# Kernel optimization log

Measured on AMD Instinct MI355X. Metric: run time of the kernel, lower is better.

## Reference

```python
import jax, jax.numpy as jnp
import numpy as np

NUM_HEADS = 8
NUM_GROUPS = 32
EPS = 1e-5


def group_norm(x, gamma, beta):
    b, c, h, w = x.shape
    xg = x.reshape(b, NUM_GROUPS, c // NUM_GROUPS, h, w)
    mean = jnp.mean(xg, axis=(2, 3, 4), keepdims=True)
    var = jnp.var(xg, axis=(2, 3, 4), keepdims=True)
    xn = ((xg - mean) * jax.lax.rsqrt(var + EPS)).reshape(b, c, h, w)
    return xn * gamma[None, :, None, None] + beta[None, :, None, None]


def setup_inputs() -> dict:
    key = jax.random.key(0)
    ks = jax.random.split(key, 4)
    b, c, h, w = 16, 512, 32, 32
    x = jax.random.normal(ks[0], (b, c, h, w), dtype=jnp.float32)
    gn_gamma = jnp.ones((c,), dtype=jnp.float32)
    gn_beta = jnp.zeros((c,), dtype=jnp.float32)
    qkv_w = jax.random.normal(ks[1], (3 * c, c), dtype=jnp.float32) * (1.0 / np.sqrt(c))
    qkv_b = jnp.zeros((3 * c,), dtype=jnp.float32)
    proj_w = jax.random.normal(ks[2], (c, c), dtype=jnp.float32) * (1.0 / np.sqrt(c))
    proj_b = jnp.zeros((c,), dtype=jnp.float32)
    return {"x": x, "gn_gamma": gn_gamma, "gn_beta": gn_beta,
            "qkv_w": qkv_w, "qkv_b": qkv_b, "proj_w": proj_w, "proj_b": proj_b}


def reference(x, gn_gamma, gn_beta, qkv_w, qkv_b, proj_w, proj_b):
    b, c, h, w = x.shape
    hd = c // NUM_HEADS
    hw = h * w

    xn = group_norm(x, gn_gamma, gn_beta)
    # 1x1 conv == channel matmul
    qkv = jnp.einsum('oc,bchw->bohw', qkv_w, xn) + qkv_b[None, :, None, None]
    q, k, v = jnp.split(qkv, 3, axis=1)
    q = q.reshape(b, NUM_HEADS, hd, hw)
    k = k.reshape(b, NUM_HEADS, hd, hw)
    v = v.reshape(b, NUM_HEADS, hd, hw)

    scale = 1.0 / np.sqrt(hd)
    attn = jnp.einsum('bhdt,bhds->bhts', q, k) * scale  # [b,H,hw,hw]
    attn = jax.nn.softmax(attn, axis=-1)
    h_attn = jnp.einsum('bhts,bhds->bhdt', attn, v).reshape(b, c, h, w)

    h_attn = jnp.einsum('oc,bchw->bohw', proj_w, h_attn) + proj_b[None, :, None, None]
    return x + h_attn
```

## Files before the change

### kernel.cpp

```cpp
#include <hip/hip_runtime.h>
#include <math.h>

#define NUM_HEADS 8
#define NUM_GROUPS 32
#define EPS 1e-5f

constexpr int B  = 16;
constexpr int C  = 512;
constexpr int HW = 1024;
constexpr int HD = 64;

typedef short bf16x8 __attribute__((ext_vector_type(8)));
typedef float f32x4  __attribute__((ext_vector_type(4)));

#define QSCALE 0.1803368801111f

__device__ inline unsigned short f2bf(float f) {
    union { float f; unsigned int u; } v; v.f = f;
    unsigned int r = (v.u + 0x7FFFu + ((v.u >> 16) & 1u)) >> 16;
    return (unsigned short)r;
}

__device__ __forceinline__ unsigned int pack_trunc(float lo, float hi) {
    return __builtin_amdgcn_perm(__float_as_uint(hi), __float_as_uint(lo), 0x07060302u);
}

__device__ __forceinline__ float exp2_raw(float x) {
#if __has_builtin(__builtin_amdgcn_exp2f)
    return __builtin_amdgcn_exp2f(x);
#else
    float r; asm("v_exp_f32 %0, %1" : "=v"(r) : "v"(x)); return r;
#endif
}

__device__ __forceinline__ void gld_lds16(void* lds, const void* g) {
    __builtin_amdgcn_global_load_lds(
        (const __attribute__((address_space(1))) void*)g,
        (__attribute__((address_space(3))) void*)lds, 16, 0, 0);
}

__device__ __forceinline__ void pl32_swap(unsigned int& a, unsigned int& b) {
#if __has_builtin(__builtin_amdgcn_permlane32_swap)
    auto r = __builtin_amdgcn_permlane32_swap(a, b, false, false);
    a = r[0]; b = r[1];
#else
    asm volatile("v_permlane32_swap_b32 %0, %1" : "+v"(a), "+v"(b));
#endif
}
__device__ __forceinline__ void pl16_swap(unsigned int& a, unsigned int& b) {
#if __has_builtin(__builtin_amdgcn_permlane16_swap)
    auto r = __builtin_amdgcn_permlane16_swap(a, b, false, false);
    a = r[0]; b = r[1];
#else
    asm volatile("v_permlane16_swap_b32 %0, %1" : "+v"(a), "+v"(b));
#endif
}

__global__ __launch_bounds__(256)
void groupnorm_t_kernel(const float* __restrict__ x,
                        const float* __restrict__ gamma,
                        const float* __restrict__ beta,
                        unsigned short* __restrict__ xnT) {
    const int bg = blockIdx.x;
    const int b = bg >> 5, g = bg & 31;
    const size_t base = ((size_t)b * C + (size_t)g * 16) * HW;

    float v[4][16];
    float sum = 0.f, sumsq = 0.f;
    #pragma unroll
    for (int p = 0; p < 4; ++p) {
        const int t = threadIdx.x + p * 256;
        #pragma unroll
        for (int cl = 0; cl < 16; ++cl) {
            const float f = x[base + (size_t)cl * HW + t];
            v[p][cl] = f;
            sum += f;
            sumsq += f * f;
        }
    }
    #pragma unroll
    for (int off = 32; off > 0; off >>= 1) {
        sum   += __shfl_down(sum, off, 64);
        sumsq += __shfl_down(sumsq, off, 64);
    }
    __shared__ float s_sum[4], s_sq[4];
    const int wid = threadIdx.x >> 6, lane = threadIdx.x & 63;
    if (lane == 0) { s_sum[wid] = sum; s_sq[wid] = sumsq; }
    __syncthreads();
    const float tsum = s_sum[0] + s_sum[1] + s_sum[2] + s_sum[3];
    const float tsq  = s_sq[0] + s_sq[1] + s_sq[2] + s_sq[3];
    const float mean = tsum * (1.0f / 16384.f);
    const float var  = tsq * (1.0f / 16384.f) - mean * mean;
    const float rstd = rsqrtf(var + EPS);

    float ga[16], be[16];
    #pragma unroll
    for (int cl = 0; cl < 16; ++cl) {
        ga[cl] = gamma[g * 16 + cl] * rstd;
        be[cl] = beta[g * 16 + cl] - mean * ga[cl];
    }

    #pragma unroll
    for (int p = 0; p < 4; ++p) {
        const int t = threadIdx.x + p * 256;
        unsigned short pk[16];
        #pragma unroll
        for (int cl = 0; cl < 16; ++cl)
            pk[cl] = f2bf(v[p][cl] * ga[cl] + be[cl]);
        unsigned short* dst = xnT + ((size_t)(b * 1024 + t)) * 512 + g * 16;
        *(uint4*)dst = *(const uint4*)pk;
        *(uint4*)(dst + 8) = *(const uint4*)(pk + 8);
    }
}

__global__ __launch_bounds__(256)
void wconv_kernel(const float* __restrict__ qkv_w,
                  const float* __restrict__ proj_w,
                  unsigned short* __restrict__ wqb) {
    const int i = blockIdx.x * 256 + threadIdx.x;
    const int n1 = 786432 / 4;
    const int nt = 1048576 / 4;
    if (i >= nt) return;
    const float4 v = (i < n1) ? ((const float4*)qkv_w)[i]
                              : ((const float4*)proj_w)[i - n1];
    ushort4 r;
    r.x = f2bf(v.x); r.y = f2bf(v.y); r.z = f2bf(v.z); r.w = f2bf(v.w);
    ((ushort4*)wqb)[i] = r;
}

__device__ __forceinline__ void mfma_gemm_core(const char* __restrict__ Ab,
                                               const char* __restrict__ Bb,
                                               unsigned short* As,
                                               unsigned short* Bs,
                                               f32x4 acc[4][4]) {
    const int tid = threadIdx.x;
    const int w = tid >> 6, lane = tid & 63;
    const int lo = lane & 15, q4 = lane >> 4;
    const int wm = w >> 1, wn = w & 1;
    const int lrow = lane >> 2, lkc = lane & 3;

    for (int k0 = 0; k0 < 512; k0 += 32) {
        __syncthreads();
        #pragma unroll
        for (int i = 0; i < 2; ++i) {
            const int row = w * 32 + i * 16 + lrow;
            const int kc = lkc ^ ((row >> 1) & 3);
            const size_t goff = (size_t)row * 1024 + k0 * 2 + kc * 16;
            gld_lds16((char*)As + w * 2048 + i * 1024, Ab + goff);
            gld_lds16((char*)Bs + w * 2048 + i * 1024, Bb + goff);
        }
        __syncthreads();

        bf16x8 af[4], bfr[4];
        #pragma unroll
        for (int i = 0; i < 4; ++i) {
            const int ra = wm * 64 + i * 16 + lo;
            af[i]  = *(const bf16x8*)(As + ra * 32 + (q4 ^ ((ra >> 1) & 3)) * 8);
            const int rb = wn * 64 + i * 16 + lo;
            bfr[i] = *(const bf16x8*)(Bs + rb * 32 + (q4 ^ ((rb >> 1) & 3)) * 8);
        }
        #pragma unroll
        for (int mi = 0; mi < 4; ++mi)
            #pragma unroll
            for (int ni = 0; ni < 4; ++ni)
                acc[mi][ni] = __builtin_amdgcn_mfma_f32_16x16x32_bf16(
                    af[mi], bfr[ni], acc[mi][ni], 0, 0, 0);
    }
}

__global__ __launch_bounds__(256)
void qkv_mfma_kernel(const unsigned short* __restrict__ wqb,
                     const unsigned short* __restrict__ xnT,
                     const float* __restrict__ qkv_b,
                     unsigned short* __restrict__ Qt,
                     unsigned short* __restrict__ Kt,
                     unsigned short* __restrict__ Vb) {
    __shared__ __align__(16) unsigned short SMEM[8192];
    unsigned short* As = SMEM;
    unsigned short* Bs = SMEM + 4096;
    const int batch = blockIdx.z;
    const int mBase = blockIdx.y * 128, nBase = blockIdx.x * 128;

    f32x4 acc[4][4] = {};
    mfma_gemm_core((const char*)(wqb + (size_t)mBase * 512),
                   (const char*)(xnT + ((size_t)batch * 1024 + nBase) * 512),
                   As, Bs, acc);

    const int tid = threadIdx.x;
    const int w = tid >> 6, lane = tid & 63;
    const int lo = lane & 15, q4 = lane >> 4;
    const int wm = w >> 1, wn = w & 1;
    const int mw = mBase + wm * 64;
    const int tb = nBase + wn * 64;

    __syncthreads();

    if (mw < 1024) {
        const bool isQ = mw < 512;
        const int head = (mw >> 6) & 7;
        unsigned short* dst = (isQ ? Qt : Kt) + (((size_t)batch * 8 + head) << 16);
        const float sc = isQ ? QSCALE : 1.0f;
        #pragma unroll
        for (int mi = 0; mi < 4; ++mi) {
            const float4 bq = *(const float4*)(qkv_b + mw + mi * 16 + q4 * 4);
            #pragma unroll
            for (int ni = 0; ni < 4; ++ni) {
                const int t = tb + ni * 16 + lo;
                ushort4 pk;
                pk.x = f2bf((acc[mi][ni][0] + bq.x) * sc);
                pk.y = f2bf((acc[mi][ni][1] + bq.y) * sc);
                pk.z = f2bf((acc[mi][ni][2] + bq.z) * sc);
                pk.w = f2bf((acc[mi][ni][3] + bq.w) * sc);
                *(ushort4*)(dst + (size_t)t * 64 + mi * 16 + q4 * 4) = pk;
            }
        }
    } else {
        unsigned short* T = SMEM + w * 2048;
        unsigned short* Vrow = Vb + (size_t)batch * 524288 + (size_t)(mw - 1024) * 1024 + tb;
        const int rl8 = lane >> 3, c8 = lane & 7;
        #pragma unroll
        for (int p = 0; p < 2; ++p) {
            #pragma unroll
            for (int mi2 = 0; mi2 < 2; ++mi2) {
                const int mi = 2 * p + mi2;
                const float4 bq = *(const float4*)(qkv_b + mw + mi * 16 + q4 * 4);
                const int dl = mi2 * 16 + q4 * 4;
                #pragma unroll
                for (int ni = 0; ni < 4; ++ni) {
                    const int tl = ni * 16 + lo;
                    T[(dl + 0) * 64 + tl] = f2bf(acc[mi][ni][0] + bq.x);
                    T[(dl + 1) * 64 + tl] = f2bf(acc[mi][ni][1] + bq.y);
                    T[(dl + 2) * 64 + tl] = f2bf(acc[mi][ni][2] + bq.z);
                    T[(dl + 3) * 64 + tl] = f2bf(acc[mi][ni][3] + bq.w);
                }
            }
            #pragma unroll
            for (int i = 0; i < 4; ++i) {
                const int dl = i * 8 + rl8;
                const uint4 val = *(const uint4*)&T[dl * 64 + c8 * 8];
                *(uint4*)(Vrow + (size_t)(p * 32 + dl) * 1024 + c8 * 8) = val;
            }
        }
    }
}

__global__ __launch_bounds__(256, 4)
void attn_mfma_kernel(const unsigned short* __restrict__ Qt,
                      const unsigned short* __restrict__ Kt,
                      const unsigned short* __restrict__ Vb,
                      unsigned short* __restrict__ attnT) {
    const int bh = blockIdx.x;
    const int b = bh >> 3, h = bh & 7;
    const int tBase = blockIdx.y * 128;
    const int tid = threadIdx.x;
    const int w = tid >> 6, lane = tid & 63;
    const int lo = lane & 15, q4 = lane >> 4;
    const int xr = lo & 7;

    __shared__ __align__(16) unsigned short Ks[2][64 * 64];
    __shared__ __align__(16) unsigned short Vs[2][64 * 64];

    const unsigned short* Kp = Kt + ((size_t)bh << 16);
    const unsigned short* Vp = Vb + ((size_t)b * 512 + h * 64) * 1024;

    bf16x8 qf[2][2];
    {
        const unsigned short* Qp = Qt + ((size_t)bh * 1024 + tBase + 32 * w) * 64;
        #pragma unroll
        for (int nt = 0; nt < 2; ++nt) {
            qf[nt][0] = *(const bf16x8*)(Qp + (size_t)(16 * nt + lo) * 64 + 8 * q4);
            qf[nt][1] = *(const bf16x8*)(Qp + (size_t)(16 * nt + lo) * 64 + 32 + 8 * q4);
        }
    }

    const int rl = lane >> 3, p8 = lane & 7;
    auto stage = [&](int s0, unsigned short* Kd, unsigned short* Vd) {
        #pragma unroll
        for (int cc = 0; cc < 2; ++cc) {
            const int r = 16 * w + 8 * cc + rl;
            const int jj = p8 ^ (r & 7);
            gld_lds16(Kd + (16 * w + 8 * cc) * 64, Kp + (size_t)(s0 + r) * 64 + jj * 8);
            gld_lds16(Vd + (16 * w + 8 * cc) * 64, Vp + (size_t)r * 1024 + s0 + jj * 8);
        }
    };

    f32x4 oacc[4][2] = {};
    float lrun[2] = {0.f, 0.f};

    auto chunk = [&](const unsigned short* Kc, const unsigned short* Vc,
                     int s0next, unsigned short* KsN, unsigned short* VsN,
                     bool doStage) {
        __syncthreads();
        if (doStage) stage(s0next, KsN, VsN);

        f32x4 sacc[4][2] = {};
        __builtin_amdgcn_s_setprio(1);
        #pragma unroll
        for (int mt = 0; mt < 4; ++mt) {
            const unsigned short* kr = Kc + (16 * mt + lo) * 64;
            const bf16x8 a0 = *(const bf16x8*)(kr + ((q4    ) ^ xr) * 8);
            const bf16x8 a1 = *(const bf16x8*)(kr + ((q4 + 4) ^ xr) * 8);
            #pragma unroll
            for (int nt = 0; nt < 2; ++nt) {
                sacc[mt][nt] = __builtin_amdgcn_mfma_f32_16x16x32_bf16(a0, qf[nt][0], sacc[mt][nt], 0, 0, 0);
                sacc[mt][nt] = __builtin_amdgcn_mfma_f32_16x16x32_bf16(a1, qf[nt][1], sacc[mt][nt], 0, 0, 0);
            }
        }
        __builtin_amdgcn_s_setprio(0);

        bf16x8 bp[2][2];
        #pragma unroll
        for (int nt = 0; nt < 2; ++nt) {
            unsigned int X[4][2];
            float ps = 0.f;
            #pragma unroll
            for (int mt = 0; mt < 4; ++mt) {
                const f32x4 s = sacc[mt][nt];
                const float p0 = exp2_raw(s[0]);
                const float p1 = exp2_raw(s[1]);
                const float p2 = exp2_raw(s[2]);
                const float p3 = exp2_raw(s[3]);
                ps += (p0 + p1) + (p2 + p3);
                X[mt][0] = pack_trunc(p0, p1);
                X[mt][1] = pack_trunc(p2, p3);
            }
            lrun[nt] += ps;
            #pragma unroll
            for (int h2 = 0; h2 < 2; ++h2) {
                unsigned int Y0, Y1, Y2, Y3;
                {
                    unsigned int a = X[2 * h2][0], bb = X[2 * h2 + 1][0];
                    pl32_swap(a, bb);
                    pl16_swap(a, bb);
                    Y0 = a; Y2 = bb;
                }
                {
                    unsigned int a = X[2 * h2][1], bb = X[2 * h2 + 1][1];
                    pl32_swap(a, bb);
                    pl16_swap(a, bb);
                    Y1 = a; Y3 = bb;
                }
                union { unsigned int u[4]; bf16x8 v; } cv;
                cv.u[0] = Y0; cv.u[1] = Y1; cv.u[2] = Y2; cv.u[3] = Y3;
                bp[nt][h2] = cv.v;
            }
        }

        __builtin_amdgcn_s_setprio(1);
        #pragma unroll
        for (int md = 0; md < 4; ++md) {
            const unsigned short* vr = Vc + (16 * md + lo) * 64;
            const bf16x8 v0 = *(const bf16x8*)(vr + ((q4    ) ^ xr) * 8);
            const bf16x8 v1 = *(const bf16x8*)(vr + ((q4 + 4) ^ xr) * 8);
            #pragma unroll
            for (int nt = 0; nt < 2; ++nt) {
                oacc[md][nt] = __builtin_amdgcn_mfma_f32_16x16x32_bf16(v0, bp[nt][0], oacc[md][nt], 0, 0, 0);
                oacc[md][nt] = __builtin_amdgcn_mfma_f32_16x16x32_bf16(v1, bp[nt][1], oacc[md][nt], 0, 0, 0);
            }
        }
        __builtin_amdgcn_s_setprio(0);
    };

    stage(0, Ks[0], Vs[0]);

    #pragma unroll 1
    for (int ii = 0; ii < 8; ++ii) {
        chunk(Ks[0], Vs[0], (2 * ii + 1) * 64, Ks[1], Vs[1], true);
        chunk(Ks[1], Vs[1], (2 * ii + 2) * 64, Ks[0], Vs[0], ii < 7);
    }

    #pragma unroll
    for (int nt = 0; nt < 2; ++nt) {
        float lt = lrun[nt];
        lt += __shfl_xor(lt, 16, 64);
        lt += __shfl_xor(lt, 32, 64);
        const float inv = 1.0f / lt;
        const int t = tBase + 32 * w + 16 * nt + lo;
        unsigned short* op = attnT + ((size_t)(b * 1024 + t)) * 512 + h * 64;
        #pragma unroll
        for (int md = 0; md < 4; ++md) {
            uint2 pk;
            pk.x = pack_trunc(oacc[md][nt][0] * inv, oacc[md][nt][1] * inv);
            pk.y = pack_trunc(oacc[md][nt][2] * inv, oacc[md][nt][3] * inv);
            *(uint2*)(op + 16 * md + 4 * q4) = pk;
        }
    }
}

__global__ __launch_bounds__(256)
void proj_mfma_kernel(const unsigned short* __restrict__ wpb,
                      const unsigned short* __restrict__ attnT,
                      const float* __restrict__ proj_b,
                      const float* __restrict__ x,
                      float* __restrict__ out) {
    __shared__ __align__(16) unsigned short As[128 * 32];
    __shared__ __align__(16) unsigned short Bs[128 * 32];
    const int batch = blockIdx.z;
    const int mBase = blockIdx.y * 128, nBase = blockIdx.x * 128;

    f32x4 acc[4][4] = {};
    mfma_gemm_core((const char*)(wpb + (size_t)mBase * 512),
                   (const char*)(attnT + ((size_t)batch * 1024 + nBase) * 512),
                   As, Bs, acc);

    const int tid = threadIdx.x;
    const int w = tid >> 6, lane = tid & 63;
    const int lo = lane & 15, q4 = lane >> 4;
    const int wm = w >> 1, wn = w & 1;
    const float* xb = x + (size_t)batch * 524288;
    float* ob = out + (size_t)batch * 524288;

    #pragma unroll
    for (int mi = 0; mi < 4; ++mi) {
        const int m0 = mBase + wm * 64 + mi * 16 + q4 * 4;
        const float4 bq = *(const float4*)(proj_b + m0);
        #pragma unroll
        for (int ni = 0; ni < 4; ++ni) {
            const int t = nBase + wn * 64 + ni * 16 + lo;
            const size_t o0 = (size_t)m0 * 1024 + t;
            ob[o0]          = acc[mi][ni][0] + bq.x + xb[o0];
            ob[o0 + 1024]   = acc[mi][ni][1] + bq.y + xb[o0 + 1024];
            ob[o0 + 2048]   = acc[mi][ni][2] + bq.z + xb[o0 + 2048];
            ob[o0 + 3072]   = acc[mi][ni][3] + bq.w + xb[o0 + 3072];
        }
    }
}

extern "C" void kernel_launch(void* const* d_in, const int* in_sizes, int n_in,
                              void* d_out, int out_size, void* d_ws, size_t ws_size,
                              hipStream_t stream) {
    const float* x        = (const float*)d_in[0];
    const float* gn_gamma = (const float*)d_in[1];
    const float* gn_beta  = (const float*)d_in[2];
    const float* qkv_w    = (const float*)d_in[3];
    const float* qkv_b    = (const float*)d_in[4];
    const float* proj_w   = (const float*)d_in[5];
    const float* proj_b   = (const float*)d_in[6];
    float* out = (float*)d_out;

    char* wsc = (char*)d_ws;
    unsigned short* xnT   = (unsigned short*)(wsc);
    unsigned short* Qt    = (unsigned short*)(wsc + 16777216);
    unsigned short* Kt    = (unsigned short*)(wsc + 33554432);
    unsigned short* Vb    = (unsigned short*)(wsc + 50331648);
    unsigned short* attnT = (unsigned short*)(wsc + 67108864);
    unsigned short* wqb   = (unsigned short*)(wsc + 83886080);
    unsigned short* wpb   = wqb + 786432;

    groupnorm_t_kernel<<<B * NUM_GROUPS, 256, 0, stream>>>(x, gn_gamma, gn_beta, xnT);

    wconv_kernel<<<1024, 256, 0, stream>>>(qkv_w, proj_w, wqb);

    {
        dim3 grid(HW / 128, (3 * C) / 128, B);
        qkv_mfma_kernel<<<grid, 256, 0, stream>>>(wqb, xnT, qkv_b, Qt, Kt, Vb);
    }

    {
        dim3 grid(B * NUM_HEADS, HW / 128);
        attn_mfma_kernel<<<grid, 256, 0, stream>>>(Qt, Kt, Vb, attnT);
    }

    {
        dim3 grid(HW / 128, C / 128, B);
        proj_mfma_kernel<<<grid, 256, 0, stream>>>(wpb, attnT, proj_b, x, out);
    }
}
```

Measured before the change: 226.0 us.

## Triple-buffer K/V staging in attention with explicit vmcnt barriers

Converts the attention kernel's double-buffered K/V LDS pipeline into a three-stage ring, so loads for chunk i+2 are in flight while chunk i is computed. The plain __syncthreads is replaced with an inline-asm s_waitcnt vmcnt(N) plus s_barrier, so each wave waits only on the oldest outstanding direct-to-LDS loads rather than draining all of them. The aim is to hide global-load latency behind MFMA work. In exchange, LDS use per block grows by half and launch bounds drop from 4 to 3 blocks per CU, which may cost occupancy. The hard-coded vmcnt count must match the number of loads per stage.

Result: faster. 212.7 us (-5.9%).

```diff
diff --git a/kernel.cpp b/kernel.cpp
--- a/kernel.cpp
+++ b/kernel.cpp
@@ -55,6 +55,11 @@
     asm volatile("v_permlane16_swap_b32 %0, %1" : "+v"(a), "+v"(b));
 #endif
 }
+
+#define ABAR(VM) do {                                                   \
+    asm volatile("s_waitcnt vmcnt(" VM ")\n\ts_barrier" ::: "memory");  \
+    __builtin_amdgcn_sched_barrier(0);                                  \
+} while (0)
 
 __global__ __launch_bounds__(256)
 void groupnorm_t_kernel(const float* __restrict__ x,
@@ -244,7 +249,94 @@
     }
 }
 
-__global__ __launch_bounds__(256, 4)
+__device__ __forceinline__ void attn_stage(const unsigned short* __restrict__ Kp,
+                                           const unsigned short* __restrict__ Vp,
+                                           int s0, unsigned short* Kd,
+                                           unsigned short* Vd,
+                                           int w, int rl, int p8) {
+    #pragma unroll
+    for (int cc = 0; cc < 2; ++cc) {
+        const int r = 16 * w + 8 * cc + rl;
+        const int jj = p8 ^ (r & 7);
+        gld_lds16(Kd + (16 * w + 8 * cc) * 64, Kp + (size_t)(s0 + r) * 64 + jj * 8);
+        gld_lds16(Vd + (16 * w + 8 * cc) * 64, Vp + (size_t)r * 1024 + s0 + jj * 8);
+    }
+}
+
+__device__ __forceinline__ void attn_chunk(const unsigned short* __restrict__ Kc,
+                                           const unsigned short* __restrict__ Vc,
+                                           const bf16x8 (&qf)[2][2],
+                                           f32x4 (&oacc)[4][2], float (&lrun)[2],
+                                           int lo, int q4, int xr) {
+    f32x4 sacc[4][2] = {};
+    __builtin_amdgcn_s_setprio(1);
+    #pragma unroll
+    for (int mt = 0; mt < 4; ++mt) {
+        const unsigned short* kr = Kc + (16 * mt + lo) * 64;
+        const bf16x8 a0 = *(const bf16x8*)(kr + ((q4    ) ^ xr) * 8);
+        const bf16x8 a1 = *(const bf16x8*)(kr + ((q4 + 4) ^ xr) * 8);
+        #pragma unroll
+        for (int nt = 0; nt < 2; ++nt) {
+            sacc[mt][nt] = __builtin_amdgcn_mfma_f32_16x16x32_bf16(a0, qf[nt][0], sacc[mt][nt], 0, 0, 0);
+            sacc[mt][nt] = __builtin_amdgcn_mfma_f32_16x16x32_bf16(a1, qf[nt][1], sacc[mt][nt], 0, 0, 0);
+        }
+    }
+    __builtin_amdgcn_s_setprio(0);
+
+    bf16x8 bp[2][2];
+    #pragma unroll
+    for (int nt = 0; nt < 2; ++nt) {
+        unsigned int X[4][2];
+        float ps = 0.f;
+        #pragma unroll
+        for (int mt = 0; mt < 4; ++mt) {
+            const f32x4 s = sacc[mt][nt];
+            const float p0 = exp2_raw(s[0]);
+            const float p1 = exp2_raw(s[1]);
+            const float p2 = exp2_raw(s[2]);
+            const float p3 = exp2_raw(s[3]);
+            ps += (p0 + p1) + (p2 + p3);
+            X[mt][0] = pack_trunc(p0, p1);
+            X[mt][1] = pack_trunc(p2, p3);
+        }
+        lrun[nt] += ps;
+        #pragma unroll
+        for (int h2 = 0; h2 < 2; ++h2) {
+            unsigned int Y0, Y1, Y2, Y3;
+            {
+                unsigned int a = X[2 * h2][0], bb = X[2 * h2 + 1][0];
+                pl32_swap(a, bb);
+                pl16_swap(a, bb);
+                Y0 = a; Y2 = bb;
+            }
+            {
+                unsigned int a = X[2 * h2][1], bb = X[2 * h2 + 1][1];
+                pl32_swap(a, bb);
+                pl16_swap(a, bb);
+                Y1 = a; Y3 = bb;
+            }
+            union { unsigned int u[4]; bf16x8 v; } cv;
+            cv.u[0] = Y0; cv.u[1] = Y1; cv.u[2] = Y2; cv.u[3] = Y3;
+            bp[nt][h2] = cv.v;
+        }
+    }
+
+    __builtin_amdgcn_s_setprio(1);
+    #pragma unroll
+    for (int md = 0; md < 4; ++md) {
+        const unsigned short* vr = Vc + (16 * md + lo) * 64;
+        const bf16x8 v0 = *(const bf16x8*)(vr + ((q4    ) ^ xr) * 8);
+        const bf16x8 v1 = *(const bf16x8*)(vr + ((q4 + 4) ^ xr) * 8);
+        #pragma unroll
+        for (int nt = 0; nt < 2; ++nt) {
+            oacc[md][nt] = __builtin_amdgcn_mfma_f32_16x16x32_bf16(v0, bp[nt][0], oacc[md][nt], 0, 0, 0);
+            oacc[md][nt] = __builtin_amdgcn_mfma_f32_16x16x32_bf16(v1, bp[nt][1], oacc[md][nt], 0, 0, 0);
+        }
+    }
+    __builtin_amdgcn_s_setprio(0);
+}
+
+__global__ __launch_bounds__(256, 3)
 void attn_mfma_kernel(const unsigned short* __restrict__ Qt,
                       const unsigned short* __restrict__ Kt,
                       const unsigned short* __restrict__ Vb,
@@ -257,8 +349,8 @@
     const int lo = lane & 15, q4 = lane >> 4;
     const int xr = lo & 7;
 
-    __shared__ __align__(16) unsigned short Ks[2][64 * 64];
-    __shared__ __align__(16) unsigned short Vs[2][64 * 64];
+    __shared__ __align__(16) unsigned short Ks[3][64 * 64];
+    __shared__ __align__(16) unsigned short Vs[3][64 * 64];
 
     const unsigned short* Kp = Kt + ((size_t)bh << 16);
     const unsigned short* Vp = Vb + ((size_t)b * 512 + h * 64) * 1024;
@@ -274,100 +366,38 @@
     }
 
     const int rl = lane >> 3, p8 = lane & 7;
-    auto stage = [&](int s0, unsigned short* Kd, unsigned short* Vd) {
-        #pragma unroll
-        for (int cc = 0; cc < 2; ++cc) {
-            const int r = 16 * w + 8 * cc + rl;
-            const int jj = p8 ^ (r & 7);
-            gld_lds16(Kd + (16 * w + 8 * cc) * 64, Kp + (size_t)(s0 + r) * 64 + jj * 8);
-            gld_lds16(Vd + (16 * w + 8 * cc) * 64, Vp + (size_t)r * 1024 + s0 + jj * 8);
-        }
-    };
 
     f32x4 oacc[4][2] = {};
     float lrun[2] = {0.f, 0.f};
 
-    auto chunk = [&](const unsigned short* Kc, const unsigned short* Vc,
-                     int s0next, unsigned short* KsN, unsigned short* VsN,
-                     bool doStage) {
-        __syncthreads();
-        if (doStage) stage(s0next, KsN, VsN);
-
-        f32x4 sacc[4][2] = {};
-        __builtin_amdgcn_s_setprio(1);
-        #pragma unroll
-        for (int mt = 0; mt < 4; ++mt) {
-            const unsigned short* kr = Kc + (16 * mt + lo) * 64;
-            const bf16x8 a0 = *(const bf16x8*)(kr + ((q4    ) ^ xr) * 8);
-            const bf16x8 a1 = *(const bf16x8*)(kr + ((q4 + 4) ^ xr) * 8);
-            #pragma unroll
-            for (int nt = 0; nt < 2; ++nt) {
-                sacc[mt][nt] = __builtin_amdgcn_mfma_f32_16x16x32_bf16(a0, qf[nt][0], sacc[mt][nt], 0, 0, 0);
-                sacc[mt][nt] = __builtin_amdgcn_mfma_f32_16x16x32_bf16(a1, qf[nt][1], sacc[mt][nt], 0, 0, 0);
-            }
-        }
-        __builtin_amdgcn_s_setprio(0);
-
-        bf16x8 bp[2][2];
-        #pragma unroll
-        for (int nt = 0; nt < 2; ++nt) {
-            unsigned int X[4][2];
-            float ps = 0.f;
-            #pragma unroll
-            for (int mt = 0; mt < 4; ++mt) {
-                const f32x4 s = sacc[mt][nt];
-                const float p0 = exp2_raw(s[0]);
-                const float p1 = exp2_raw(s[1]);
-                const float p2 = exp2_raw(s[2]);
-                const float p3 = exp2_raw(s[3]);
-                ps += (p0 + p1) + (p2 + p3);
-                X[mt][0] = pack_trunc(p0, p1);
-                X[mt][1] = pack_trunc(p2, p3);
-            }
-            lrun[nt] += ps;
-            #pragma unroll
-            for (int h2 = 0; h2 < 2; ++h2) {
-                unsigned int Y0, Y1, Y2, Y3;
-                {
-                    unsigned int a = X[2 * h2][0], bb = X[2 * h2 + 1][0];
-                    pl32_swap(a, bb);
-                    pl16_swap(a, bb);
-                    Y0 = a; Y2 = bb;
-                }
-                {
-                    unsigned int a = X[2 * h2][1], bb = X[2 * h2 + 1][1];
-                    pl32_swap(a, bb);
-                    pl16_swap(a, bb);
-                    Y1 = a; Y3 = bb;
-                }
-                union { unsigned int u[4]; bf16x8 v; } cv;
-                cv.u[0] = Y0; cv.u[1] = Y1; cv.u[2] = Y2; cv.u[3] = Y3;
-                bp[nt][h2] = cv.v;
-            }
-        }
-
-        __builtin_amdgcn_s_setprio(1);
-        #pragma unroll
-        for (int md = 0; md < 4; ++md) {
-            const unsigned short* vr = Vc + (16 * md + lo) * 64;
-            const bf16x8 v0 = *(const bf16x8*)(vr + ((q4    ) ^ xr) * 8);
-            const bf16x8 v1 = *(const bf16x8*)(vr + ((q4 + 4) ^ xr) * 8);
-            #pragma unroll
-            for (int nt = 0; nt < 2; ++nt) {
-                oacc[md][nt] = __builtin_amdgcn_mfma_f32_16x16x32_bf16(v0, bp[nt][0], oacc[md][nt], 0, 0, 0);
-                oacc[md][nt] = __builtin_amdgcn_mfma_f32_16x16x32_bf16(v1, bp[nt][1], oacc[md][nt], 0, 0, 0);
-            }
-        }
-        __builtin_amdgcn_s_setprio(0);
-    };
-
-    stage(0, Ks[0], Vs[0]);
+    attn_stage(Kp, Vp, 0 * 64, Ks[0], Vs[0], w, rl, p8);
+    attn_stage(Kp, Vp, 1 * 64, Ks[1], Vs[1], w, rl, p8);
+
+    ABAR("4");
+    attn_stage(Kp, Vp, 2 * 64, Ks[2], Vs[2], w, rl, p8);
+    attn_chunk(Ks[0], Vs[0], qf, oacc, lrun, lo, q4, xr);
 
     #pragma unroll 1
-    for (int ii = 0; ii < 8; ++ii) {
-        chunk(Ks[0], Vs[0], (2 * ii + 1) * 64, Ks[1], Vs[1], true);
-        chunk(Ks[1], Vs[1], (2 * ii + 2) * 64, Ks[0], Vs[0], ii < 7);
-    }
+    for (int ii = 0; ii < 4; ++ii) {
+        const int i = 3 * ii + 1;
+        ABAR("4");
+        attn_stage(Kp, Vp, (i + 2) * 64, Ks[0], Vs[0], w, rl, p8);
+        attn_chunk(Ks[1], Vs[1], qf, oacc, lrun, lo, q4, xr);
+        ABAR("4");
+        attn_stage(Kp, Vp, (i + 3) * 64, Ks[1], Vs[1], w, rl, p8);
+        attn_chunk(Ks[2], Vs[2], qf, oacc, lrun, lo, q4, xr);
+        ABAR("4");
+        attn_stage(Kp, Vp, (i + 4) * 64, Ks[2], Vs[2], w, rl, p8);
+        attn_chunk(Ks[0], Vs[0], qf, oacc, lrun, lo, q4, xr);
+    }
+
+    ABAR("4");
+    attn_stage(Kp, Vp, 15 * 64, Ks[0], Vs[0], w, rl, p8);
+    attn_chunk(Ks[1], Vs[1], qf, oacc, lrun, lo, q4, xr);
+    ABAR("4");
+    attn_chunk(Ks[2], Vs[2], qf, oacc, lrun, lo, q4, xr);
+    ABAR("0");
+    attn_chunk(Ks[0], Vs[0], qf, oacc, lrun, lo, q4, xr);
 
     #pragma unroll
     for (int nt = 0; nt < 2; ++nt) {
```
